# Kernel optimization log

Hardware: AMD Instinct MI355X
Metric: run time of the kernel (lower is better)

## Reference

```python
import jax, jax.numpy as jnp
import numpy as np

NUM_HEADS = 16


def setup_inputs() -> dict:
    key = jax.random.key(0)
    k1, k2, k3 = jax.random.split(key, 3)
    B, S, E = 2, 2048, 1024
    hidden_states = jax.random.normal(k1, (B, S, E), dtype=jnp.float32)
    c_attn_w = jax.random.normal(k2, (E, 3 * E), dtype=jnp.float32) * 0.02
    c_attn_b = jnp.zeros((3 * E,), dtype=jnp.float32)
    c_proj_w = jax.random.normal(k3, (E, E), dtype=jnp.float32) * 0.02
    c_proj_b = jnp.zeros((E,), dtype=jnp.float32)
    return {
        "hidden_states": hidden_states,
        "c_attn_w": c_attn_w,
        "c_attn_b": c_attn_b,
        "c_proj_w": c_proj_w,
        "c_proj_b": c_proj_b,
    }


def reference(hidden_states, c_attn_w, c_attn_b, c_proj_w, c_proj_b):
    B, S, E = hidden_states.shape
    H = NUM_HEADS
    D = E // H
    # Conv1D: qkv projection -> [B, S, 3E]
    qkv = jnp.einsum("bse,ef->bsf", hidden_states, c_attn_w) + c_attn_b
    q, k, v = jnp.split(qkv, 3, axis=-1)
    # split heads -> [B, H, S, D]
    def heads(x):
        return x.reshape(B, S, H, D).transpose(0, 2, 1, 3)
    q, k, v = heads(q), heads(k), heads(v)
    # scaled QK^T -> [B, H, S, S]
    scale = jnp.asarray(D, dtype=q.dtype) ** 0.5
    attn_weights = jnp.einsum("bhqd,bhkd->bhqk", q, k) / scale
    # causal mask (bias buffer): True on/below diagonal
    causal = jnp.tril(jnp.ones((S, S), dtype=bool))
    mask_value = jnp.finfo(attn_weights.dtype).min
    attn_weights = jnp.where(causal[None, None, :, :], attn_weights, mask_value)
    attn_weights = jax.nn.softmax(attn_weights, axis=-1)
    # attn @ V -> merge heads -> [B, S, E]
    attn_out = jnp.einsum("bhqk,bhkd->bhqd", attn_weights, v)
    attn_out = attn_out.transpose(0, 2, 1, 3).reshape(B, S, E)
    # output projection (Conv1D)
    out = jnp.einsum("bse,ef->bsf", attn_out, c_proj_w) + c_proj_b
    return out
```

## Files before the change

### kernel.cpp

```cpp
#include <hip/hip_runtime.h>
#include <stdint.h>

typedef __attribute__((ext_vector_type(8))) __bf16 bf16x8;
typedef __attribute__((ext_vector_type(4))) __bf16 bf16x4;
typedef __attribute__((ext_vector_type(4))) float f32x4;

#define MFMA16(a, b, c) __builtin_amdgcn_mfma_f32_16x16x32_bf16(a, b, c, 0, 0, 0)

__device__ __forceinline__ void async_ld16(const __bf16* g, __bf16* lds_base) {
    __builtin_amdgcn_global_load_lds(
        (const __attribute__((address_space(1))) void*)g,
        (__attribute__((address_space(3))) void*)lds_base, 16, 0, 0);
}

__global__ __launch_bounds__(256) void k_prep(
    const float* __restrict__ hs, const float* __restrict__ w1,
    const float* __restrict__ w2, __bf16* __restrict__ hsb,
    __bf16* __restrict__ w1t, __bf16* __restrict__ w2t) {
    __shared__ __bf16 tile[32][33];
    int bid = blockIdx.x, tid = threadIdx.x;
    if (bid < 4096) {
        int i = (bid * 256 + tid) * 4;
        float4 v = *(const float4*)(hs + i);
        bf16x4 o;
        o.x = (__bf16)v.x; o.y = (__bf16)v.y; o.z = (__bf16)v.z; o.w = (__bf16)v.w;
        *(bf16x4*)(hsb + i) = o;
        return;
    }
    const float* in; __bf16* out; int C, tb;
    if (bid < 7168) { in = w1; out = w1t; C = 3072; tb = bid - 4096; }
    else            { in = w2; out = w2t; C = 1024; tb = bid - 7168; }
    const int R = 1024;
    int ntc = C >> 5;
    int c0 = (tb % ntc) * 32, r0 = (tb / ntc) * 32;
    int tx = tid & 31, ty = tid >> 5;
#pragma unroll
    for (int i = 0; i < 4; i++)
        tile[ty + i * 8][tx] = (__bf16)in[(size_t)(r0 + ty + i * 8) * C + c0 + tx];
    __syncthreads();
#pragma unroll
    for (int i = 0; i < 4; i++)
        out[(size_t)(c0 + ty + i * 8) * R + r0 + tx] = tile[tx][ty + i * 8];
}

__global__ __launch_bounds__(256, 3) void k_gemm_qkv(
    const __bf16* __restrict__ A, const __bf16* __restrict__ Bt,
    const float* __restrict__ bias,
    __bf16* __restrict__ Qo, __bf16* __restrict__ Ko, __bf16* __restrict__ Vo) {
    __shared__ __bf16 As[128 * 64];
    __shared__ __bf16 Bs[128 * 64];
    const int Kd = 1024;
    int lid = blockIdx.x;
    int xcd = lid & 7, c = lid >> 3;
    int mi = (xcd >> 1) * 8 + c / 12;
    int ni = (xcd & 1) * 12 + c % 12;
    int n0 = ni * 128, m0 = mi * 128;
    bool tr = (ni < 16);
    int tid = threadIdx.x;
    int wv = tid >> 6, lane = tid & 63;
    int wm = (wv >> 1) * 64, wn = (wv & 1) * 64;
    int quad = lane >> 4, l16 = lane & 15;
    int rl = lane >> 3, sj = lane & 7;
    int sgo = (sj ^ rl) << 3;
    int swl = l16 & 7;
    const __bf16* p0 = tr ? Bs : As;
    const __bf16* p1 = tr ? As : Bs;
    int o0 = tr ? wn : wm, o1 = tr ? wm : wn;
    f32x4 acc[4][4] = {};
    for (int k0 = 0; k0 < Kd; k0 += 64) {
        __syncthreads();
#pragma unroll
        for (int r = 0; r < 4; r++) {
            int row = wv * 32 + r * 8;
            async_ld16(&A[(size_t)(m0 + row + rl) * Kd + k0 + sgo], &As[row * 64]);
            async_ld16(&Bt[(size_t)(n0 + row + rl) * Kd + k0 + sgo], &Bs[row * 64]);
        }
        __syncthreads();
#pragma unroll
        for (int ks = 0; ks < 2; ks++) {
            bf16x8 f0[4], f1[4];
#pragma unroll
            for (int i = 0; i < 4; i++)
                f0[i] = *(const bf16x8*)(
                    &p0[(o0 + i * 16 + l16) * 64 + (((ks * 4 + quad) ^ swl) << 3)]);
#pragma unroll
            for (int j = 0; j < 4; j++)
                f1[j] = *(const bf16x8*)(
                    &p1[(o1 + j * 16 + l16) * 64 + (((ks * 4 + quad) ^ swl) << 3)]);
#pragma unroll
            for (int i = 0; i < 4; i++)
#pragma unroll
                for (int j = 0; j < 4; j++)
                    acc[i][j] = MFMA16(f0[i], f1[j], acc[i][j]);
        }
    }
    if (tr) {
#pragma unroll
        for (int i = 0; i < 4; i++) {
#pragma unroll
            for (int j = 0; j < 4; j++) {
                int nb = n0 + wn + i * 16 + quad * 4;
                int sec = nb >> 10, nl = nb & 1023;
                int h = nl >> 6, d = nl & 63;
                int sg = m0 + wm + j * 16 + l16;
                int bb = sg >> 11, s = sg & 2047;
                f32x4 bv = *(const f32x4*)(&bias[nb]);
                __bf16* dst = (sec == 0) ? Qo : Ko;
                float scl = (sec == 0) ? 0.1803368801f : 1.0f;
                bf16x4 q4;
#pragma unroll
                for (int r = 0; r < 4; r++)
                    q4[r] = (__bf16)((acc[i][j][r] + bv[r]) * scl);
                *(bf16x4*)(&dst[((size_t)(bb * 16 + h) * 2048 + s) * 64 + d]) = q4;
            }
        }
    } else {
#pragma unroll
        for (int i = 0; i < 4; i++) {
#pragma unroll
            for (int j = 0; j < 4; j++) {
                int n = n0 + wn + j * 16 + l16;
                float bv = bias[n];
                int nl = n & 1023;
                int h = nl >> 6, d = nl & 63;
                int mbase = m0 + wm + i * 16 + quad * 4;
                int bb = mbase >> 11, s = mbase & 2047;
                bf16x4 v4;
#pragma unroll
                for (int r = 0; r < 4; r++) v4[r] = (__bf16)(acc[i][j][r] + bv);
                *(bf16x4*)(&Vo[((size_t)(bb * 16 + h) * 64 + d) * 2048 + s]) = v4;
            }
        }
    }
}

__global__ __launch_bounds__(256, 3) void k_gemm_proj(
    const __bf16* __restrict__ A, const __bf16* __restrict__ Bt,
    const float* __restrict__ bias, float* __restrict__ out) {
    __shared__ __bf16 As[64 * 64];
    __shared__ __bf16 Bs[128 * 64];
    const int Kd = 1024;
    int lid = blockIdx.x;
    int xcd = lid & 7, c = lid >> 3;
    int mi = xcd * 8 + (c >> 3);
    int ni = c & 7;
    int n0 = ni * 128, m0 = mi * 64;
    int tid = threadIdx.x;
    int wv = tid >> 6, lane = tid & 63;
    int wm = (wv >> 1) * 32, wn = (wv & 1) * 64;
    int quad = lane >> 4, l16 = lane & 15;
    int rl = lane >> 3, sj = lane & 7;
    int sgo = (sj ^ rl) << 3;
    int swl = l16 & 7;
    f32x4 acc[4][2] = {};
    for (int k0 = 0; k0 < Kd; k0 += 64) {
        __syncthreads();
#pragma unroll
        for (int r = 0; r < 2; r++) {
            int row = wv * 16 + r * 8;
            async_ld16(&A[(size_t)(m0 + row + rl) * Kd + k0 + sgo], &As[row * 64]);
        }
#pragma unroll
        for (int r = 0; r < 4; r++) {
            int row = wv * 32 + r * 8;
            async_ld16(&Bt[(size_t)(n0 + row + rl) * Kd + k0 + sgo], &Bs[row * 64]);
        }
        __syncthreads();
#pragma unroll
        for (int ks = 0; ks < 2; ks++) {
            bf16x8 f0[4], f1[2];
#pragma unroll
            for (int i = 0; i < 4; i++)
                f0[i] = *(const bf16x8*)(
                    &Bs[(wn + i * 16 + l16) * 64 + (((ks * 4 + quad) ^ swl) << 3)]);
#pragma unroll
            for (int j = 0; j < 2; j++)
                f1[j] = *(const bf16x8*)(
                    &As[(wm + j * 16 + l16) * 64 + (((ks * 4 + quad) ^ swl) << 3)]);
#pragma unroll
            for (int i = 0; i < 4; i++)
#pragma unroll
                for (int j = 0; j < 2; j++)
                    acc[i][j] = MFMA16(f0[i], f1[j], acc[i][j]);
        }
    }
#pragma unroll
    for (int i = 0; i < 4; i++) {
#pragma unroll
        for (int j = 0; j < 2; j++) {
            int nb = n0 + wn + i * 16 + quad * 4;
            int m = m0 + wm + j * 16 + l16;
            f32x4 bv = *(const f32x4*)(&bias[nb]);
            f32x4 o = acc[i][j] + bv;
            *(f32x4*)(&out[(size_t)m * 1024 + nb]) = o;
        }
    }
}

__device__ const int ATT_ORDER[24] = {7, 8, 10, 12, 14, 16, 18, 20, 22, 23, 6, 21,
                                      5, 19, 4, 17, 3, 15, 2, 13, 1, 11, 0, 9};

__global__ __launch_bounds__(256, 3) void k_attn(
    const __bf16* __restrict__ Qg, const __bf16* __restrict__ Kg,
    const __bf16* __restrict__ Vtg, __bf16* __restrict__ Op, float* __restrict__ Lp) {
    __shared__ __bf16 Ksb[2][64 * 64];
    __shared__ __bf16 Vtb[2][64 * 64];
    __shared__ __bf16 Ps[128 * 72];
    int bh = blockIdx.x & 31;
    int slot = ATT_ORDER[blockIdx.x >> 5];
    int t, k0, k1;
    if (slot < 8) { t = slot; k0 = 0; k1 = 2 * t + 2; }
    else { int i2 = slot - 8; t = 8 + (i2 >> 1); k0 = (i2 & 1) * 16; k1 = min(k0 + 16, 2 * t + 2); }
    const __bf16* Qp = Qg + (size_t)bh * 2048 * 64;
    const __bf16* Kp = Kg + (size_t)bh * 2048 * 64;
    const __bf16* Vp = Vtg + (size_t)bh * 64 * 2048;
    int tid = threadIdx.x, wv = tid >> 6, lane = tid & 63;
    int quad = lane >> 4, l16 = lane & 15;
    int rl = lane >> 3, sj = lane & 7;
    int sgo = (sj ^ rl) << 3;
    int swl = l16 & 7;

    bf16x8 qf[2][2];
#pragma unroll
    for (int qn = 0; qn < 2; qn++)
#pragma unroll
        for (int ks = 0; ks < 2; ks++)
            qf[qn][ks] = *(const bf16x8*)(
                &Qp[(size_t)(t * 128 + wv * 32 + qn * 16 + l16) * 64 + ks * 32 + quad * 8]);
    const f32x4 zf = {0.f, 0.f, 0.f, 0.f};
    f32x4 lacc[2] = {zf, zf};
    f32x4 acc_o[2][4] = {};
    int qwmax = t * 128 + wv * 32 + 31;

    auto stage = [&](int buf, int kt) {
#pragma unroll
        for (int half = 0; half < 2; half++) {
            int r0 = wv * 16 + half * 8;
            async_ld16(&Kp[(size_t)(kt * 64 + r0 + rl) * 64 + sgo], &Ksb[buf][r0 * 64]);
            async_ld16(&Vp[(size_t)(r0 + rl) * 2048 + kt * 64 + sgo], &Vtb[buf][r0 * 64]);
        }
    };

    stage(0, k0);
    __syncthreads();

    for (int kt = k0; kt < k1; kt++) {
        int cur = (kt - k0) & 1;
        if (kt + 1 < k1) stage(cur ^ 1, kt + 1);
        if (kt * 64 <= qwmax) {
            const __bf16* Kc = Ksb[cur];
            const __bf16* Vc = Vtb[cur];
            f32x4 s[2][4];
#pragma unroll
            for (int ks = 0; ks < 2; ks++) {
                bf16x8 kf[4];
#pragma unroll
                for (int i = 0; i < 4; i++)
                    kf[i] = *(const bf16x8*)(
                        &Kc[(i * 16 + l16) * 64 + (((ks * 4 + quad) ^ swl) << 3)]);
                __builtin_amdgcn_s_setprio(1);
#pragma unroll
                for (int i = 0; i < 4; i++)
#pragma unroll
                    for (int qn = 0; qn < 2; qn++)
                        s[qn][i] = MFMA16(kf[i], qf[qn][ks], ks == 0 ? zf : s[qn][i]);
                __builtin_amdgcn_s_setprio(0);
            }
#pragma unroll
            for (int qn = 0; qn < 2; qn++) {
                int qmin = t * 128 + wv * 32 + qn * 16;
                if (kt * 64 + 63 > qmin) {
#pragma unroll
                    for (int i = 0; i < 4; i++)
#pragma unroll
                        for (int r = 0; r < 4; r++)
                            if (kt * 64 + i * 16 + quad * 4 + r > qmin + l16) s[qn][i][r] = -1e30f;
                }
            }
#pragma unroll
            for (int qn = 0; qn < 2; qn++)
#pragma unroll
                for (int i = 0; i < 4; i++) {
                    f32x4 pe;
#pragma unroll
                    for (int r = 0; r < 4; r++) pe[r] = exp2f(s[qn][i][r]);
                    lacc[qn] += pe;
                    bf16x4 pk;
#pragma unroll
                    for (int r = 0; r < 4; r++) pk[r] = (__bf16)pe[r];
                    *(bf16x4*)(&Ps[(wv * 32 + qn * 16 + l16) * 72 + i * 16 + quad * 4]) = pk;
                }
#pragma unroll
            for (int ks = 0; ks < 2; ks++) {
                bf16x8 pf[2];
#pragma unroll
                for (int qn = 0; qn < 2; qn++)
                    pf[qn] = *(const bf16x8*)(
                        &Ps[(wv * 32 + qn * 16 + l16) * 72 + ks * 32 + quad * 8]);
                bf16x8 vf[4];
#pragma unroll
                for (int i = 0; i < 4; i++)
                    vf[i] = *(const bf16x8*)(
                        &Vc[(i * 16 + l16) * 64 + (((ks * 4 + quad) ^ swl) << 3)]);
                __builtin_amdgcn_s_setprio(1);
#pragma unroll
                for (int i = 0; i < 4; i++)
#pragma unroll
                    for (int qn = 0; qn < 2; qn++)
                        acc_o[qn][i] = MFMA16(vf[i], pf[qn], acc_o[qn][i]);
                __builtin_amdgcn_s_setprio(0);
            }
        }
        __syncthreads();
    }
    size_t pbase = (size_t)slot * 32 + bh;
#pragma unroll
    for (int qn = 0; qn < 2; qn++) {
        float ls = lacc[qn][0] + lacc[qn][1] + lacc[qn][2] + lacc[qn][3];
        ls += __shfl_xor(ls, 16);
        ls += __shfl_xor(ls, 32);
        int ql = wv * 32 + qn * 16 + l16;
        if (quad == 0) Lp[pbase * 128 + ql] = ls;
#pragma unroll
        for (int i = 0; i < 4; i++) {
            bf16x4 o4;
#pragma unroll
            for (int r = 0; r < 4; r++) o4[r] = (__bf16)acc_o[qn][i][r];
            *(bf16x4*)(&Op[(pbase * 128 + ql) * 64 + i * 16 + quad * 4]) = o4;
        }
    }
}

__global__ __launch_bounds__(256) void k_attn_combine(
    const __bf16* __restrict__ Op, const float* __restrict__ Lp,
    __bf16* __restrict__ AOb) {
    int gid = blockIdx.x * 256 + threadIdx.x;
    int d4 = gid & 15;
    int q = (gid >> 4) & 2047;
    int bh = gid >> 15;
    int t = q >> 7, ql = q & 127;
    int n = (t <= 7) ? 1 : 2;
    int base = (t <= 7) ? t : 8 + 2 * (t - 8);
    float L = 0.f, o[4] = {};
    for (int c = 0; c < n; c++) {
        size_t idx = (size_t)(base + c) * 32 + bh;
        L += Lp[idx * 128 + ql];
        bf16x4 p4 = *(const bf16x4*)(&Op[(idx * 128 + ql) * 64 + d4 * 4]);
#pragma unroll
        for (int r = 0; r < 4; r++) o[r] += (float)p4[r];
    }
    float inv = 1.f / L;
    int b = bh >> 4, h = bh & 15;
    bf16x4 o4;
#pragma unroll
    for (int r = 0; r < 4; r++) o4[r] = (__bf16)(o[r] * inv);
    *(bf16x4*)(&AOb[((size_t)b * 2048 + q) * 1024 + h * 64 + d4 * 4]) = o4;
}

extern "C" void kernel_launch(void* const* d_in, const int* in_sizes, int n_in,
                              void* d_out, int out_size, void* d_ws, size_t ws_size,
                              hipStream_t stream) {
    const float* hs = (const float*)d_in[0];
    const float* w1 = (const float*)d_in[1];
    const float* b1 = (const float*)d_in[2];
    const float* w2 = (const float*)d_in[3];
    const float* b2 = (const float*)d_in[4];
    float* out = (float*)d_out;

    char* ws = (char*)d_ws;
    __bf16* hsb = (__bf16*)(ws);
    __bf16* w1t = (__bf16*)(ws + (size_t)8 * 1024 * 1024);
    __bf16* w2t = (__bf16*)(ws + (size_t)14 * 1024 * 1024);
    __bf16* Qb  = (__bf16*)(ws + (size_t)16 * 1024 * 1024);
    __bf16* Kb  = (__bf16*)(ws + (size_t)24 * 1024 * 1024);
    __bf16* Vb  = (__bf16*)(ws + (size_t)32 * 1024 * 1024);
    __bf16* AOb = (__bf16*)(ws + (size_t)40 * 1024 * 1024);
    __bf16* Opart = (__bf16*)(ws);
    float*  Lpart = (float*)(ws + (size_t)13 * 1024 * 1024);

    k_prep<<<8192, 256, 0, stream>>>(hs, w1, w2, hsb, w1t, w2t);
    k_gemm_qkv<<<768, 256, 0, stream>>>(hsb, w1t, b1, Qb, Kb, Vb);
    k_attn<<<768, 256, 0, stream>>>(Qb, Kb, Vb, Opart, Lpart);
    k_attn_combine<<<4096, 256, 0, stream>>>(Opart, Lpart, AOb);
    k_gemm_proj<<<512, 256, 0, stream>>>(AOb, w2t, b2, out);
}
```

Before: 181.0 us.

## Compute softmax row sums via MFMA and normalize unsplit tiles in attention kernel

Row-sum accumulation of exp values moves from VALU adds plus cross-lane shuffles to an extra MFMA against a ones vector, so every lane ends up holding the row sum. Query tiles that are not split (t<8) now normalize and write straight into the merged-head output, skipping the partial buffers. The combine kernel is cut down to handle only the split tiles with half the grid. The sum is now taken from bf16-rounded probabilities, and two extra MFMAs are added per k-step.

```diff
diff --git a/kernel.cpp b/kernel.cpp
--- a/kernel.cpp
+++ b/kernel.cpp
@@ -202,7 +202,8 @@
 
 __global__ __launch_bounds__(256, 3) void k_attn(
     const __bf16* __restrict__ Qg, const __bf16* __restrict__ Kg,
-    const __bf16* __restrict__ Vtg, __bf16* __restrict__ Op, float* __restrict__ Lp) {
+    const __bf16* __restrict__ Vtg, __bf16* __restrict__ Op, float* __restrict__ Lp,
+    __bf16* __restrict__ AOb) {
     __shared__ __bf16 Ksb[2][64 * 64];
     __shared__ __bf16 Vtb[2][64 * 64];
     __shared__ __bf16 Ps[128 * 72];
@@ -228,7 +229,9 @@
             qf[qn][ks] = *(const bf16x8*)(
                 &Qp[(size_t)(t * 128 + wv * 32 + qn * 16 + l16) * 64 + ks * 32 + quad * 8]);
     const f32x4 zf = {0.f, 0.f, 0.f, 0.f};
-    f32x4 lacc[2] = {zf, zf};
+    const __bf16 one1 = (__bf16)1.0f;
+    const bf16x8 onesv = {one1, one1, one1, one1, one1, one1, one1, one1};
+    f32x4 acc_l[2] = {zf, zf};
     f32x4 acc_o[2][4] = {};
     int qwmax = t * 128 + wv * 32 + 31;
 
@@ -281,13 +284,9 @@
             for (int qn = 0; qn < 2; qn++)
 #pragma unroll
                 for (int i = 0; i < 4; i++) {
-                    f32x4 pe;
-#pragma unroll
-                    for (int r = 0; r < 4; r++) pe[r] = exp2f(s[qn][i][r]);
-                    lacc[qn] += pe;
                     bf16x4 pk;
 #pragma unroll
-                    for (int r = 0; r < 4; r++) pk[r] = (__bf16)pe[r];
+                    for (int r = 0; r < 4; r++) pk[r] = (__bf16)exp2f(s[qn][i][r]);
                     *(bf16x4*)(&Ps[(wv * 32 + qn * 16 + l16) * 72 + i * 16 + quad * 4]) = pk;
                 }
 #pragma unroll
@@ -308,25 +307,43 @@
 #pragma unroll
                     for (int qn = 0; qn < 2; qn++)
                         acc_o[qn][i] = MFMA16(vf[i], pf[qn], acc_o[qn][i]);
+#pragma unroll
+                for (int qn = 0; qn < 2; qn++)
+                    acc_l[qn] = MFMA16(onesv, pf[qn], acc_l[qn]);
                 __builtin_amdgcn_s_setprio(0);
             }
         }
         __syncthreads();
     }
-    size_t pbase = (size_t)slot * 32 + bh;
-#pragma unroll
-    for (int qn = 0; qn < 2; qn++) {
-        float ls = lacc[qn][0] + lacc[qn][1] + lacc[qn][2] + lacc[qn][3];
-        ls += __shfl_xor(ls, 16);
-        ls += __shfl_xor(ls, 32);
-        int ql = wv * 32 + qn * 16 + l16;
-        if (quad == 0) Lp[pbase * 128 + ql] = ls;
-#pragma unroll
-        for (int i = 0; i < 4; i++) {
-            bf16x4 o4;
-#pragma unroll
-            for (int r = 0; r < 4; r++) o4[r] = (__bf16)acc_o[qn][i][r];
-            *(bf16x4*)(&Op[(pbase * 128 + ql) * 64 + i * 16 + quad * 4]) = o4;
+    if (slot < 8) {
+        int b = bh >> 4, h = bh & 15;
+#pragma unroll
+        for (int qn = 0; qn < 2; qn++) {
+            float inv = 1.f / acc_l[qn][0];
+            int q = t * 128 + wv * 32 + qn * 16 + l16;
+#pragma unroll
+            for (int i = 0; i < 4; i++) {
+                bf16x4 o4;
+#pragma unroll
+                for (int r = 0; r < 4; r++) o4[r] = (__bf16)(acc_o[qn][i][r] * inv);
+                *(bf16x4*)(&AOb[((size_t)b * 2048 + q) * 1024 + h * 64 +
+                                i * 16 + quad * 4]) = o4;
+            }
+        }
+    } else {
+        size_t pbase = (size_t)slot * 32 + bh;
+#pragma unroll
+        for (int qn = 0; qn < 2; qn++) {
+            float ls = acc_l[qn][0];
+            int ql = wv * 32 + qn * 16 + l16;
+            if (quad == 0) Lp[pbase * 128 + ql] = ls;
+#pragma unroll
+            for (int i = 0; i < 4; i++) {
+                bf16x4 o4;
+#pragma unroll
+                for (int r = 0; r < 4; r++) o4[r] = (__bf16)acc_o[qn][i][r];
+                *(bf16x4*)(&Op[(pbase * 128 + ql) * 64 + i * 16 + quad * 4]) = o4;
+            }
         }
     }
 }
@@ -336,13 +353,13 @@
     __bf16* __restrict__ AOb) {
     int gid = blockIdx.x * 256 + threadIdx.x;
     int d4 = gid & 15;
-    int q = (gid >> 4) & 2047;
-    int bh = gid >> 15;
+    int q = 1024 + ((gid >> 4) & 1023);
+    int bh = gid >> 14;
     int t = q >> 7, ql = q & 127;
-    int n = (t <= 7) ? 1 : 2;
-    int base = (t <= 7) ? t : 8 + 2 * (t - 8);
+    int base = 8 + 2 * (t - 8);
     float L = 0.f, o[4] = {};
-    for (int c = 0; c < n; c++) {
+#pragma unroll
+    for (int c = 0; c < 2; c++) {
         size_t idx = (size_t)(base + c) * 32 + bh;
         L += Lp[idx * 128 + ql];
         bf16x4 p4 = *(const bf16x4*)(&Op[(idx * 128 + ql) * 64 + d4 * 4]);
@@ -380,7 +397,7 @@
 
     k_prep<<<8192, 256, 0, stream>>>(hs, w1, w2, hsb, w1t, w2t);
     k_gemm_qkv<<<768, 256, 0, stream>>>(hsb, w1t, b1, Qb, Kb, Vb);
-    k_attn<<<768, 256, 0, stream>>>(Qb, Kb, Vb, Opart, Lpart);
-    k_attn_combine<<<4096, 256, 0, stream>>>(Opart, Lpart, AOb);
+    k_attn<<<768, 256, 0, stream>>>(Qb, Kb, Vb, Opart, Lpart, AOb);
+    k_attn_combine<<<2048, 256, 0, stream>>>(Opart, Lpart, AOb);
     k_gemm_proj<<<512, 256, 0, stream>>>(AOb, w2t, b2, out);
 }
```

Result: faster. 171.7 us (median of 2 runs) (-5.1%).
